# Kernel optimization log

Measured on AMD Instinct MI355X. Metric: run time of the kernel, lower is better.

Reference implementation:

```python
import jax, jax.numpy as jnp
import numpy as np

NEG_SLOPE = 0.2
EPS = 1e-16

N_NODES = 50000
N_EDGES = 800000
IN_DIM = 64
HEADS = 4
HEAD_DIM = 64


def setup_inputs() -> dict:
    key = jax.random.key(0)
    k1, k2, k3, k4, k5 = jax.random.split(key, 5)
    x = jax.random.normal(k1, (N_NODES, IN_DIM), dtype=jnp.float32)
    edge_index = jax.random.randint(k2, (2, N_EDGES), 0, N_NODES, dtype=jnp.int64)
    W = jax.random.normal(k3, (IN_DIM, HEADS * HEAD_DIM), dtype=jnp.float32) * (1.0 / np.sqrt(IN_DIM))
    att_src = jax.random.normal(k4, (HEADS, HEAD_DIM), dtype=jnp.float32) * 0.1
    att_dst = jax.random.normal(k5, (HEADS, HEAD_DIM), dtype=jnp.float32) * 0.1
    bias = jnp.zeros((HEADS * HEAD_DIM,), dtype=jnp.float32)
    return {"x": x, "edge_index": edge_index, "W": W,
            "att_src": att_src, "att_dst": att_dst, "bias": bias}


def reference(x, edge_index, W, att_src, att_dst, bias):
    N = x.shape[0]
    H, D = att_src.shape
    # add self-loops (PyG default add_self_loops=True)
    loop = jnp.arange(N, dtype=edge_index.dtype)
    src = jnp.concatenate([edge_index[0], loop])  # message source j
    dst = jnp.concatenate([edge_index[1], loop])  # message target i

    h = (x @ W).reshape(N, H, D)                 # [N,H,D] per-head projection
    a_src = jnp.einsum('nhd,hd->nh', h, att_src)  # [N,H]
    a_dst = jnp.einsum('nhd,hd->nh', h, att_dst)  # [N,H]

    score = jax.nn.leaky_relu(a_src[src] + a_dst[dst], NEG_SLOPE)  # [E,H]
    # segment softmax over edges grouped by destination node
    m = jax.ops.segment_max(score, dst, num_segments=N)            # [N,H]
    m = jnp.where(jnp.isfinite(m), m, 0.0)
    e = jnp.exp(score - m[dst])                                    # [E,H]
    denom = jax.ops.segment_sum(e, dst, num_segments=N)            # [N,H]
    alpha = e / (denom[dst] + EPS)                                 # [E,H]

    msgs = h[src] * alpha[:, :, None]                              # [E,H,D]
    out = jax.ops.segment_sum(msgs, dst, num_segments=N)           # [N,H,D]
    return out.reshape(N, H * D) + bias
```

## Files before the change

kernel.cpp:

```cpp
#include <hip/hip_runtime.h>

#define N_NODES 50000
#define N_EDGES 800000
#define E_TOT   850000
#define HD      256
#define MAXDEG  64
#define NEG_SLOPE 0.2f
#define EPS 1e-16f

typedef __attribute__((ext_vector_type(8))) short short8;
typedef __attribute__((ext_vector_type(4))) float f32x4;

__device__ __forceinline__ unsigned short f2bf(float f) {
    union { float f; unsigned int i; } c; c.f = f;
    unsigned int r = 0x7fffu + ((c.i >> 16) & 1u);
    return (unsigned short)((c.i + r) >> 16);
}
__device__ __forceinline__ short8 pack8(float4 a, float4 b) {
    short8 r;
    r[0] = (short)f2bf(a.x); r[1] = (short)f2bf(a.y);
    r[2] = (short)f2bf(a.z); r[3] = (short)f2bf(a.w);
    r[4] = (short)f2bf(b.x); r[5] = (short)f2bf(b.y);
    r[6] = (short)f2bf(b.z); r[7] = (short)f2bf(b.w);
    return r;
}
__device__ __forceinline__ float lrelu_exp(float v) {
    v = (v < 0.f) ? v * NEG_SLOPE : v;
    return __expf(v);
}

__global__ __launch_bounds__(256) void prep_kernel(
        const float* __restrict__ W, const float* __restrict__ att_src,
        const float* __restrict__ att_dst, float* __restrict__ ws, float* __restrict__ wd) {
    const int t = threadIdx.x, head = t >> 6, k = t & 63;
    const float* wrow = W + k * 256 + head * 64;
    const float* as = att_src + head * 64;
    const float* adv = att_dst + head * 64;
    float s = 0.f, d = 0.f;
#pragma unroll 8
    for (int j = 0; j < 64; ++j) { s += wrow[j] * as[j]; d += wrow[j] * adv[j]; }
    ws[k * 4 + head] = s;
    wd[k * 4 + head] = d;
}

__global__ __launch_bounds__(256) void logit_bucket_kernel(
        const float* __restrict__ x,
        const float4* __restrict__ ws4, const float4* __restrict__ wd4,
        const int* __restrict__ eidx, int* __restrict__ cnt, int* __restrict__ slot,
        float4* __restrict__ a_src4, float4* __restrict__ a_dst4) {
    const int g = blockIdx.x * 256 + threadIdx.x;
    if (g < E_TOT) {
        int s, d;
        if (g < N_EDGES) { s = eidx[g]; d = eidx[N_EDGES + g]; }
        else             { s = d = g - N_EDGES; }
        int pos = atomicAdd(&cnt[d], 1);
        if (pos < MAXDEG) slot[d * MAXDEG + pos] = s;
    }

    if (g < N_NODES) {
        const float4* xr = (const float4*)(x + (size_t)g * 64);
        float4 vs = {0.f, 0.f, 0.f, 0.f};
        float4 vd = {0.f, 0.f, 0.f, 0.f};
#pragma unroll 4
        for (int kk = 0; kk < 16; ++kk) {
            float4 xv = xr[kk];
#pragma unroll
            for (int j = 0; j < 4; ++j) {
                const float xj = j == 0 ? xv.x : j == 1 ? xv.y : j == 2 ? xv.z : xv.w;
                const float4 w1 = ws4[kk * 4 + j];
                const float4 w2 = wd4[kk * 4 + j];
                vs.x += xj * w1.x; vs.y += xj * w1.y; vs.z += xj * w1.z; vs.w += xj * w1.w;
                vd.x += xj * w2.x; vd.y += xj * w2.y; vd.z += xj * w2.z; vd.w += xj * w2.w;
            }
        }
        a_src4[g] = vs;
        a_dst4[g] = vd;
    }
}

__global__ __launch_bounds__(256) void aggregate_x_kernel(
        const int* __restrict__ cnt, const int* __restrict__ slot,
        const float4* __restrict__ a_src4, const float4* __restrict__ a_dst4,
        const float* __restrict__ x, unsigned short* __restrict__ yb) {
    __shared__ int    lsrc[4][64];
    __shared__ float4 lscs[4][64];
    const int w    = threadIdx.x >> 6;
    const int lane = threadIdx.x & 63;
    const int node = blockIdx.x * 4 + w;
    int deg = cnt[node];
    if (deg > MAXDEG) deg = MAXDEG;
    const int base = node * MAXDEG;
    const float4 ad = a_dst4[node];

    int s = (lane < deg) ? slot[base + lane] : 0;
    float4 A = a_src4[s];
    float4 sc;
    if (lane < deg) {
        sc.x = lrelu_exp(A.x + ad.x); sc.y = lrelu_exp(A.y + ad.y);
        sc.z = lrelu_exp(A.z + ad.z); sc.w = lrelu_exp(A.w + ad.w);
    } else {
        sc = (float4){0.f, 0.f, 0.f, 0.f};
    }
    lsrc[w][lane] = s;
    lscs[w][lane] = sc;

    float4 ds = sc;
#pragma unroll
    for (int m = 1; m < 64; m <<= 1) {
        ds.x += __shfl_xor(ds.x, m, 64); ds.y += __shfl_xor(ds.y, m, 64);
        ds.z += __shfl_xor(ds.z, m, 64); ds.w += __shfl_xor(ds.w, m, 64);
    }
    float4 inv;
    inv.x = 1.f / (ds.x + EPS); inv.y = 1.f / (ds.y + EPS);
    inv.z = 1.f / (ds.z + EPS); inv.w = 1.f / (ds.w + EPS);

    float4 acc = {0.f, 0.f, 0.f, 0.f};
    int e = 0;
    for (; e + 3 < deg; e += 4) {
        int s0 = lsrc[w][e + 0], s1 = lsrc[w][e + 1];
        int s2 = lsrc[w][e + 2], s3 = lsrc[w][e + 3];
        float4 c0 = lscs[w][e + 0], c1 = lscs[w][e + 1];
        float4 c2 = lscs[w][e + 2], c3 = lscs[w][e + 3];
        float x0 = x[(size_t)s0 * 64 + lane];
        float x1 = x[(size_t)s1 * 64 + lane];
        float x2 = x[(size_t)s2 * 64 + lane];
        float x3 = x[(size_t)s3 * 64 + lane];
        acc.x += x0 * c0.x + x1 * c1.x + x2 * c2.x + x3 * c3.x;
        acc.y += x0 * c0.y + x1 * c1.y + x2 * c2.y + x3 * c3.y;
        acc.z += x0 * c0.z + x1 * c1.z + x2 * c2.z + x3 * c3.z;
        acc.w += x0 * c0.w + x1 * c1.w + x2 * c2.w + x3 * c3.w;
    }
    for (; e < deg; ++e) {
        int se = lsrc[w][e];
        float4 ce = lscs[w][e];
        float xv = x[(size_t)se * 64 + lane];
        acc.x += xv * ce.x; acc.y += xv * ce.y;
        acc.z += xv * ce.z; acc.w += xv * ce.w;
    }
    unsigned short* yp = yb + (size_t)node * 256 + lane;
    yp[  0] = f2bf(acc.x * inv.x);
    yp[ 64] = f2bf(acc.y * inv.y);
    yp[128] = f2bf(acc.z * inv.z);
    yp[192] = f2bf(acc.w * inv.w);
}

__global__ __launch_bounds__(256) void gemm_out_kernel(
        const unsigned short* __restrict__ yb, const float* __restrict__ W,
        const float* __restrict__ bias, float* __restrict__ out) {
    __shared__ __align__(16) unsigned short Wt[256 * 64];
    const int t = threadIdx.x;
    {
        const int c = t;
        for (int kg = 0; kg < 8; ++kg) {
            float4 lo, hi;
            lo.x = W[(kg * 8 + 0) * 256 + c]; lo.y = W[(kg * 8 + 1) * 256 + c];
            lo.z = W[(kg * 8 + 2) * 256 + c]; lo.w = W[(kg * 8 + 3) * 256 + c];
            hi.x = W[(kg * 8 + 4) * 256 + c]; hi.y = W[(kg * 8 + 5) * 256 + c];
            hi.z = W[(kg * 8 + 6) * 256 + c]; hi.w = W[(kg * 8 + 7) * 256 + c];
            *(short8*)&Wt[c * 64 + ((kg ^ (c & 7)) << 3)] = pack8(lo, hi);
        }
    }
    __syncthreads();

    const int wave = t >> 6, lane = t & 63;
    const int q = lane >> 4, mloc = lane & 15;
    const int rowbase = blockIdx.x * 64 + wave * 16;
    int arow = rowbase + mloc;
    if (arow > N_NODES - 1) arow = N_NODES - 1;

    short8 a0[4], a1[4];
#pragma unroll
    for (int h = 0; h < 4; ++h) {
        const unsigned short* yr = yb + (size_t)arow * 256 + h * 64;
        a0[h] = *(const short8*)&yr[q * 8];
        a1[h] = *(const short8*)&yr[32 + q * 8];
    }

    f32x4 acc[16];
#pragma unroll
    for (int n = 0; n < 16; ++n) acc[n] = (f32x4){0.f, 0.f, 0.f, 0.f};
#pragma unroll
    for (int n = 0; n < 16; ++n) {
        const int c = n * 16 + mloc;
        const int h = n >> 2;
        const unsigned short* rowp = &Wt[c * 64];
        short8 b0 = *(const short8*)&rowp[((q    ) ^ (c & 7)) << 3];
        short8 b1 = *(const short8*)&rowp[((4 + q) ^ (c & 7)) << 3];
        acc[n] = __builtin_amdgcn_mfma_f32_16x16x32_bf16(a0[h], b0, acc[n], 0, 0, 0);
        acc[n] = __builtin_amdgcn_mfma_f32_16x16x32_bf16(a1[h], b1, acc[n], 0, 0, 0);
    }

    float bv[16];
#pragma unroll
    for (int n = 0; n < 16; ++n) bv[n] = bias[n * 16 + mloc];

    const int orow = rowbase + q * 4;
#pragma unroll
    for (int r = 0; r < 4; ++r) {
        if (orow + r < N_NODES) {
            float* op = out + (size_t)(orow + r) * 256 + mloc;
#pragma unroll
            for (int n = 0; n < 16; ++n) op[n * 16] = acc[n][r] + bv[n];
        }
    }
}

extern "C" void kernel_launch(void* const* d_in, const int* in_sizes, int n_in,
                              void* d_out, int out_size, void* d_ws, size_t ws_size,
                              hipStream_t stream) {
    const float* x       = (const float*)d_in[0];
    const int*   eidx    = (const int*)  d_in[1];
    const float* W       = (const float*)d_in[2];
    const float* att_src = (const float*)d_in[3];
    const float* att_dst = (const float*)d_in[4];
    const float* bias    = (const float*)d_in[5];
    float* out = (float*)d_out;

    unsigned short* yb = (unsigned short*)d_ws;
    float* a_src = (float*)(yb + (size_t)N_NODES * HD);
    float* a_dst = a_src + N_NODES * 4;
    float* ws    = a_dst + N_NODES * 4;
    float* wd    = ws + 256;
    int*   cnt   = (int*)(wd + 256);
    int*   slot  = cnt + N_NODES;

    hipMemsetAsync(cnt, 0, N_NODES * sizeof(int), stream);
    prep_kernel<<<1, 256, 0, stream>>>(W, att_src, att_dst, ws, wd);
    logit_bucket_kernel<<<(E_TOT + 255) / 256, 256, 0, stream>>>(
        x, (const float4*)ws, (const float4*)wd, eidx, cnt, slot,
        (float4*)a_src, (float4*)a_dst);
    aggregate_x_kernel<<<N_NODES / 4, 256, 0, stream>>>(
        cnt, slot, (const float4*)a_src, (const float4*)a_dst, x, yb);
    gemm_out_kernel<<<(N_NODES + 63) / 64, 256, 0, stream>>>(yb, W, bias, out);
}
```

Baseline: 180.5 us.

## Replace global per-node atomic bucketing with two-pass binned ELL build

Edge bucketing no longer does one global atomicAdd per edge on a per-node counter. Each block now builds a shared-memory histogram over 98 coarse destination bins and reserves space with one global atomic per bin. Edges are scattered into a per-bin arena, and a second kernel builds each bin's ELL slots using shared-memory atomics. Source indices are stored as 16-bit values to halve slot traffic. This adds a kernel launch and an arena pass, relies on N<65536, and caps bins at CAP entries, which could drop edges under skewed inputs.

```diff
diff --git a/kernel.cpp b/kernel.cpp
--- a/kernel.cpp
+++ b/kernel.cpp
@@ -7,6 +7,12 @@
 #define MAXDEG  64
 #define NEG_SLOPE 0.2f
 #define EPS 1e-16f
+
+#define NB     98
+#define BSHIFT 9
+#define CAP    10240
+#define ABLK   392
+#define EPB    2304
 
 typedef __attribute__((ext_vector_type(8))) short short8;
 typedef __attribute__((ext_vector_type(4))) float f32x4;
@@ -43,20 +49,51 @@
     wd[k * 4 + head] = d;
 }
 
-__global__ __launch_bounds__(256) void logit_bucket_kernel(
+__global__ __launch_bounds__(256) void bin_logit_kernel(
         const float* __restrict__ x,
         const float4* __restrict__ ws4, const float4* __restrict__ wd4,
-        const int* __restrict__ eidx, int* __restrict__ cnt, int* __restrict__ slot,
+        const int* __restrict__ eidx,
+        int* __restrict__ gcnt, unsigned int* __restrict__ arena,
         float4* __restrict__ a_src4, float4* __restrict__ a_dst4) {
-    const int g = blockIdx.x * 256 + threadIdx.x;
-    if (g < E_TOT) {
-        int s, d;
-        if (g < N_EDGES) { s = eidx[g]; d = eidx[N_EDGES + g]; }
-        else             { s = d = g - N_EDGES; }
-        int pos = atomicAdd(&cnt[d], 1);
-        if (pos < MAXDEG) slot[d * MAXDEG + pos] = s;
-    }
-
+    __shared__ int hist[NB];
+    __shared__ int abase[NB];
+    const int t = threadIdx.x;
+    const int e0 = blockIdx.x * EPB;
+    if (t < NB) hist[t] = 0;
+    __syncthreads();
+
+#pragma unroll
+    for (int k = 0; k < EPB / 256; ++k) {
+        const int g = e0 + k * 256 + t;
+        if (g < E_TOT) {
+            const int d = (g < N_EDGES) ? eidx[N_EDGES + g] : g - N_EDGES;
+            atomicAdd(&hist[d >> BSHIFT], 1);
+        }
+    }
+    __syncthreads();
+    if (t < NB) {
+        const int c = hist[t];
+        abase[t] = c ? atomicAdd(&gcnt[t], c) : 0;
+        hist[t] = 0;
+    }
+    __syncthreads();
+
+#pragma unroll
+    for (int k = 0; k < EPB / 256; ++k) {
+        const int g = e0 + k * 256 + t;
+        if (g < E_TOT) {
+            int s, d;
+            if (g < N_EDGES) { s = eidx[g]; d = eidx[N_EDGES + g]; }
+            else             { s = d = g - N_EDGES; }
+            const int b = d >> BSHIFT;
+            const int pos = abase[b] + atomicAdd(&hist[b], 1);
+            if (pos < CAP)
+                arena[b * CAP + pos] =
+                    (unsigned int)s | ((unsigned int)(d & 511) << 16);
+        }
+    }
+
+    const int g = blockIdx.x * 256 + t;
     if (g < N_NODES) {
         const float4* xr = (const float4*)(x + (size_t)g * 64);
         float4 vs = {0.f, 0.f, 0.f, 0.f};
@@ -78,8 +115,31 @@
     }
 }
 
+__global__ __launch_bounds__(512) void ell_build_kernel(
+        const int* __restrict__ gcnt, const unsigned int* __restrict__ arena,
+        int* __restrict__ cnt, unsigned short* __restrict__ slotu) {
+    __shared__ int lcnt[512];
+    const int t = threadIdx.x;
+    const int b = blockIdx.x;
+    lcnt[t] = 0;
+    __syncthreads();
+    int m = gcnt[b]; if (m > CAP) m = CAP;
+    const int n0 = b << BSHIFT;
+    const unsigned int* ap = arena + (size_t)b * CAP;
+    for (int i = t; i < m; i += 512) {
+        const unsigned int p = ap[i];
+        const int dl = p >> 16;
+        const int s  = p & 0xFFFFu;
+        const int pos = atomicAdd(&lcnt[dl], 1);
+        if (pos < MAXDEG) slotu[(size_t)(n0 + dl) * MAXDEG + pos] = (unsigned short)s;
+    }
+    __syncthreads();
+    const int n = n0 + t;
+    if (n < N_NODES) cnt[n] = lcnt[t];
+}
+
 __global__ __launch_bounds__(256) void aggregate_x_kernel(
-        const int* __restrict__ cnt, const int* __restrict__ slot,
+        const int* __restrict__ cnt, const unsigned short* __restrict__ slotu,
         const float4* __restrict__ a_src4, const float4* __restrict__ a_dst4,
         const float* __restrict__ x, unsigned short* __restrict__ yb) {
     __shared__ int    lsrc[4][64];
@@ -89,10 +149,10 @@
     const int node = blockIdx.x * 4 + w;
     int deg = cnt[node];
     if (deg > MAXDEG) deg = MAXDEG;
-    const int base = node * MAXDEG;
+    const size_t base = (size_t)node * MAXDEG;
     const float4 ad = a_dst4[node];
 
-    int s = (lane < deg) ? slot[base + lane] : 0;
+    int s = (lane < deg) ? (int)slotu[base + lane] : 0;
     float4 A = a_src4[s];
     float4 sc;
     if (lane < deg) {
@@ -222,14 +282,17 @@
     float* ws    = a_dst + N_NODES * 4;
     float* wd    = ws + 256;
     int*   cnt   = (int*)(wd + 256);
-    int*   slot  = cnt + N_NODES;
-
-    hipMemsetAsync(cnt, 0, N_NODES * sizeof(int), stream);
+    int*   gcnt  = cnt + N_NODES;
+    unsigned int*   arena = (unsigned int*)(gcnt + 128);
+    unsigned short* slotu = (unsigned short*)(arena + NB * CAP);
+
+    hipMemsetAsync(gcnt, 0, 128 * sizeof(int), stream);
     prep_kernel<<<1, 256, 0, stream>>>(W, att_src, att_dst, ws, wd);
-    logit_bucket_kernel<<<(E_TOT + 255) / 256, 256, 0, stream>>>(
-        x, (const float4*)ws, (const float4*)wd, eidx, cnt, slot,
+    bin_logit_kernel<<<ABLK, 256, 0, stream>>>(
+        x, (const float4*)ws, (const float4*)wd, eidx, gcnt, arena,
         (float4*)a_src, (float4*)a_dst);
+    ell_build_kernel<<<NB, 512, 0, stream>>>(gcnt, arena, cnt, slotu);
     aggregate_x_kernel<<<N_NODES / 4, 256, 0, stream>>>(
-        cnt, slot, (const float4*)a_src, (const float4*)a_dst, x, yb);
+        cnt, slotu, (const float4*)a_src, (const float4*)a_dst, x, yb);
     gemm_out_kernel<<<(N_NODES + 63) / 64, 256, 0, stream>>>(yb, W, bias, out);
 }
```

Measured after the change: 167.7 us. 7.1% less time.
